# Optimization experiments

Measured on AMD Instinct MI355X. Metric: run time of the kernel, lower is better.

Reference implementation:

```python
import jax, jax.numpy as jnp
import numpy as np

C_IN, C_OUT, K = 64, 64, 3
KK = K * K


def _conv3x3(x, w, b):
    # x: [B, Cin, H, W], w: [Cout, Cin, 3, 3], b: [Cout] or None. stride 1, pad 1.
    y = jax.lax.conv_general_dilated(
        x, w, window_strides=(1, 1), padding=((1, 1), (1, 1)),
        dimension_numbers=("NCHW", "OIHW", "NCHW"))
    if b is not None:
        y = y + b[None, :, None, None]
    return y


def _deform_conv2d(x, offset, mask, weight):
    # torchvision.ops.deform_conv2d with stride=1, pad=1, dilation=1, 1 offset group.
    # x: [B,C,H,W]; offset: [B,2*KK,H,W] (per-tap (dy,dx)); mask: [B,KK,H,W];
    # weight: [O,C,K,K]
    B, C, H, W = x.shape
    O = weight.shape[0]
    ky, kx = jnp.meshgrid(jnp.arange(K), jnp.arange(K), indexing="ij")
    hs = jnp.arange(H)
    ws = jnp.arange(W)
    # base sample positions per tap k=(ky*K+kx): [KK,H,W]
    base_y = (hs[:, None] - 1)[None] + ky.reshape(KK, 1, 1)
    base_x = (ws[None, :] - 1)[None] + kx.reshape(KK, 1, 1)
    off = offset.reshape(B, KK, 2, H, W)
    py = base_y[None].astype(x.dtype) + off[:, :, 0]  # [B,KK,H,W]
    px = base_x[None].astype(x.dtype) + off[:, :, 1]

    y0 = jnp.floor(py)
    x0 = jnp.floor(px)
    wy = py - y0  # bilinear fractional weights
    wx = px - x0
    y0i = y0.astype(jnp.int32)
    x0i = x0.astype(jnp.int32)

    imflat = x.reshape(B, C, H * W)

    def gather_b(im, idx):  # im: [C,HW], idx: [KK,H,W] -> [C,KK,H,W]
        return im[:, idx]

    val = jnp.zeros((B, C, KK, H, W), x.dtype)
    for dy, dx in ((0, 0), (0, 1), (1, 0), (1, 1)):
        yc = y0i + dy
        xc = x0i + dx
        valid = ((yc >= 0) & (yc < H) & (xc >= 0) & (xc < W)).astype(x.dtype)
        cw = (wy if dy else (1.0 - wy)) * (wx if dx else (1.0 - wx)) * valid
        idx = jnp.clip(yc, 0, H - 1) * W + jnp.clip(xc, 0, W - 1)
        g = jax.vmap(gather_b)(imflat, idx)  # [B,C,KK,H,W]
        val = val + cw[:, None] * g
    val = val * mask[:, None]  # modulation
    # contract 9-tap patches with conv weight
    return jnp.einsum("bckhw,ock->bohw", val, weight.reshape(O, C, KK))


def setup_inputs() -> dict:
    key = jax.random.key(0)
    ks = jax.random.split(key, 8)
    B, H, W = 4, 96, 96
    cin2 = 2 * C_IN + 2
    frame_i = jax.random.normal(ks[0], (B, C_IN, H, W), jnp.float32)
    frame_j = jax.random.normal(ks[1], (B, C_IN, H, W), jnp.float32)
    flow_ij = jax.random.normal(ks[2], (B, 2, H, W), jnp.float32)
    # small random weights so offsets are nonzero (zero-init would degenerate)
    w_off = jax.random.normal(ks[3], (2 * KK, cin2, K, K), jnp.float32) * 0.01
    b_off = jax.random.normal(ks[4], (2 * KK,), jnp.float32) * 0.1
    w_mod = jax.random.normal(ks[5], (KK, cin2, K, K), jnp.float32) * 0.01
    b_mod = jax.random.normal(ks[6], (KK,), jnp.float32) * 0.1
    w_reg = jax.random.normal(ks[7], (C_OUT, C_IN, K, K), jnp.float32) * (1.0 / np.sqrt(C_IN * KK))
    return {"frame_i": frame_i, "frame_j": frame_j, "flow_ij": flow_ij,
            "w_off": w_off, "b_off": b_off, "w_mod": w_mod, "b_mod": b_mod,
            "w_reg": w_reg}


def reference(frame_i, frame_j, flow_ij, w_off, b_off, w_mod, b_mod, w_reg):
    offset_input = jnp.concatenate([frame_i, frame_j, flow_ij], axis=1)
    offset = _conv3x3(offset_input, w_off, b_off)            # [B,2*KK,H,W]
    modulator = 2.0 * jax.nn.sigmoid(_conv3x3(offset_input, w_mod, b_mod))  # [B,KK,H,W]
    return _deform_conv2d(frame_j, offset, modulator, w_reg)
```

## Files before the change

### kernel.cpp

```cpp
#include <hip/hip_runtime.h>
#include <math.h>

#define BB   4
#define HH   96
#define WW   96
#define HW   (HH * WW)
#define CIN  64
#define COUT 64
#define NPL  17
#define HWP  (HW + 1)
#define NROW (BB * HW)
#define NSTRIP (NROW / 16)
#define BPX3 (NSTRIP / 8)
#define NA   (9 * 5 * 2 * 512)
#define NW   (9 * 2 * 4 * 512)
#define PXB2 (NROW / 32)
#define PWBLK 324
#define TSX  35
#define NIT  (NPL * 54)

typedef short v8s __attribute__((ext_vector_type(8)));
typedef float v4f __attribute__((ext_vector_type(4)));

__device__ __forceinline__ unsigned short f2bf(float f) {
    unsigned u = __float_as_uint(f);
    return (unsigned short)((u + 0x7FFFu + ((u >> 16) & 1u)) >> 16);
}
__device__ __forceinline__ unsigned pack2(float a, float b) {
    return (unsigned)f2bf(a) | ((unsigned)f2bf(b) << 16);
}
__device__ __forceinline__ unsigned bil2(unsigned a, unsigned b, unsigned c,
                                         unsigned d, float w00, float w01,
                                         float w10, float w11) {
    float lo = w00 * __uint_as_float(a << 16) + w01 * __uint_as_float(b << 16)
             + w10 * __uint_as_float(c << 16) + w11 * __uint_as_float(d << 16);
    float hi = w00 * __uint_as_float(a & 0xffff0000u)
             + w01 * __uint_as_float(b & 0xffff0000u)
             + w10 * __uint_as_float(c & 0xffff0000u)
             + w11 * __uint_as_float(d & 0xffff0000u);
    return pack2(lo, hi);
}

__global__ __launch_bounds__(256) void prep_kernel(
    const float* __restrict__ fi, const float* __restrict__ fj,
    const float* __restrict__ fl, const float* __restrict__ w_off,
    const float* __restrict__ w_mod, const float* __restrict__ w_reg,
    uint4* __restrict__ xp, unsigned short* __restrict__ wa2f,
    unsigned short* __restrict__ wb2f)
{
    int blk = blockIdx.x;
    if (blk < PXB2) {
        __shared__ __align__(16) unsigned tile[64 * TSX];
        int tid = threadIdx.x;
        int p = tid & 63, cg = tid >> 6;
        int u = blk >> 1, half = blk & 1;
        int r0 = u * 64;
        int b = r0 / HW;
        int hwb = r0 - b * HW;
        int hw = hwb + p;
        uint4* xpb = xp + (size_t)b * NPL * HWP;
        if (half == 0) {
            const float* pi = fi + (size_t)b * CIN * HW + hw;
#pragma unroll
            for (int d = 0; d < 8; ++d) {
                int c = cg * 16 + 2 * d;
                tile[p * TSX + cg * 8 + d] =
                    pack2(pi[(size_t)c * HW], pi[(size_t)(c + 1) * HW]);
            }
            __syncthreads();
#pragma unroll
            for (int i = 0; i < 2; ++i) {
                int it = i * 256 + tid;
                int pl = it >> 6, rl = it & 63;
                const unsigned* s = &tile[rl * TSX + pl * 4];
                uint4 v = {s[0], s[1], s[2], s[3]};
                xpb[(size_t)pl * HWP + hwb + rl] = v;
            }
        } else {
            const float* pj = fj + (size_t)b * CIN * HW + hw;
#pragma unroll
            for (int d = 0; d < 8; ++d) {
                int c = cg * 16 + 2 * d;
                tile[p * TSX + cg * 8 + d] =
                    pack2(pj[(size_t)c * HW], pj[(size_t)(c + 1) * HW]);
            }
            if (cg == 0) {
                const float* pf = fl + (size_t)b * 2 * HW + hw;
                tile[p * TSX + 32] = pack2(pf[0], pf[HW]);
            }
            __syncthreads();
#pragma unroll
            for (int i = 0; i < 2; ++i) {
                int it = i * 256 + tid;
                int pl = it >> 6, rl = it & 63;
                int o  = (pl >> 1) + (pl & 1) * 4;
                const unsigned* s = &tile[rl * TSX + o * 4];
                uint4 v = {s[0], s[1], s[2], s[3]};
                xpb[(size_t)(8 + pl) * HWP + hwb + rl] = v;
            }
            if (tid < 64) {
                uint4 v = {tile[tid * TSX + 32], 0u, 0u, 0u};
                xpb[(size_t)16 * HWP + hwb + tid] = v;
            }
        }
    } else if (blk < PXB2 + PWBLK) {
        int e = (blk - PXB2) * 256 + threadIdx.x;
        if (e < NA) {
            int t  = e / 5120;
            int r1 = e - t * 5120;
            int ks = r1 >> 10;
            int r2 = r1 & 1023;
            int nt = r2 >> 9;
            int l9 = r2 & 511;
            int l  = l9 >> 3, ee = l9 & 7;
            int m  = l & 15, g = l >> 4;
            int oc = nt * 16 + m;
            int ch = ks * 32 + g * 8 + ee;
            float v = 0.0f;
            if (oc < 27 && ch < 130) {
                if (oc < 18) v = w_off[((size_t)oc * 130 + ch) * 9 + t];
                else         v = w_mod[((size_t)(oc - 18) * 130 + ch) * 9 + t];
            }
            wa2f[e] = f2bf(v);
        } else {
            int e2 = e - NA;
            if (e2 < NW) {
                int k  = e2 >> 12;
                int r1 = e2 & 4095;
                int ks = r1 >> 11;
                int r2 = r1 & 2047;
                int nt = r2 >> 9;
                int l9 = r2 & 511;
                int l  = l9 >> 3, ee = l9 & 7;
                int m  = l & 15, g = l >> 4;
                int o  = nt * 16 + m;
                int c  = ks * 32 + g * 8 + ee;
                wb2f[e2] = f2bf(w_reg[((size_t)o * 64 + c) * 9 + k]);
            }
        }
    } else {
        if (threadIdx.x < BB * NPL) {
            int bz = threadIdx.x / NPL, pl = threadIdx.x - bz * NPL;
            uint4 z = {0u, 0u, 0u, 0u};
            xp[((size_t)bz * NPL + pl) * HWP + HW] = z;
        }
    }
}

__global__ __launch_bounds__(512, 8) void fused_kernel(
    const uint4* __restrict__ xp,
    const unsigned short* __restrict__ wa2f,
    const unsigned short* __restrict__ wb2f,
    const float* __restrict__ b_off, const float* __restrict__ b_mod,
    float* __restrict__ out)
{
    __shared__ __align__(16) unsigned char pool[16384];
    __shared__ __align__(16) float red1[8][8][64];
    __shared__ float lraw[16 * 28];

    uint4* patchL = (uint4*)pool;
    float* red2   = (float*)pool;

    int tid = threadIdx.x;
    int l = tid & 63;
    int wid = __builtin_amdgcn_readfirstlane(tid >> 6);
    int m = l & 15, g = l >> 4;
    int strip = (blockIdx.x & 7) * BPX3 + (blockIdx.x >> 3);
    int b = strip / (HW / 16);
    int hw0 = (strip - b * (HW / 16)) * 16;
    int hw = hw0 + m;
    int x = hw % WW, y = hw / WW;
    int y0b = hw0 / WW, x0b = hw0 - y0b * WW;

    const uint4* xpb = xp + (size_t)b * NPL * HWP;

#pragma unroll
    for (int i = 0; i < 2; ++i) {
        int item = i * 512 + tid;
        if (item < NIT) {
            int pl  = item / 54;
            int rm  = item - pl * 54;
            int run = rm / 18;
            int r18 = rm - run * 18;
            int yy = y0b + run - 1;
            int xx = x0b - 1 + r18;
            bool ok = ((unsigned)yy < HH) && ((unsigned)xx < WW);
            int pos = ok ? (yy * WW + xx) : HW;
            patchL[item] = xpb[(size_t)pl * HWP + pos];
        }
    }
    __syncthreads();

    v4f acc0 = {0.f, 0.f, 0.f, 0.f};
    v4f acc1 = {0.f, 0.f, 0.f, 0.f};
    {
        int nu = (wid < 5) ? 6 : 5;
#pragma unroll
        for (int i = 0; i < 6; ++i) {
            if (i < nu) {
                int u = wid + 8 * i;
                int t = u / 5, ks = u - 5 * t;
                int r = (t / 3) * 18 + (t % 3) + m;
                v8s a;
                if (ks == 4) {
                    uint4 t4 = patchL[16 * 54 + r];
                    if (g) t4 = (uint4){0u, 0u, 0u, 0u};
                    a = __builtin_bit_cast(v8s, t4);
                } else {
                    int pl = (ks == 0) ? g : (ks == 1) ? 4 + g
                           : (ks == 2) ? 8 + 2 * g : 9 + 2 * g;
                    a = *(const v8s*)&patchL[pl * 54 + r];
                }
                const unsigned short* wp =
                    wa2f + ((size_t)(u * 2)) * 512 + l * 8;
                v8s b0 = *(const v8s*)(wp);
                v8s b1 = *(const v8s*)(wp + 512);
                acc0 = __builtin_amdgcn_mfma_f32_16x16x32_bf16(a, b0, acc0, 0, 0, 0);
                acc1 = __builtin_amdgcn_mfma_f32_16x16x32_bf16(a, b1, acc1, 0, 0, 0);
            }
        }
    }

    {
#pragma unroll
        for (int j = 0; j < 4; ++j) red1[wid][j][l] = acc0[j];
#pragma unroll
        for (int j = 0; j < 4; ++j) red1[wid][4 + j][l] = acc1[j];
    }
    __syncthreads();

    {
        int j = wid;
        float v = 0.f;
#pragma unroll
        for (int sw = 0; sw < 8; ++sw) v += red1[sw][j][l];
        int r = j & 3;
        int oc = (j < 4) ? m : 16 + m;
        int pos = g * 4 + r;
        if (oc < 18) {
            lraw[pos * 28 + oc] = v + b_off[oc];
        } else if (oc < 27) {
            lraw[pos * 28 + oc] =
                2.0f / (1.0f + __expf(-(v + b_mod[oc - 18])));
        }
    }
    __syncthreads();

    v4f acc[4];
#pragma unroll
    for (int nt = 0; nt < 4; ++nt) acc[nt] = (v4f){0.f, 0.f, 0.f, 0.f};

    auto do_tap = [&](int k) {
        int ky = k / 3, kx = k - 3 * ky;
        float dy = lraw[m * 28 + 2 * k];
        float dx = lraw[m * 28 + 2 * k + 1];
        float mm = lraw[m * 28 + 18 + k];

        float py = (float)(y - 1 + ky) + dy;
        float px = (float)(x - 1 + kx) + dx;
        float fy = floorf(py), fx = floorf(px);
        int   y0 = (int)fy,    x0 = (int)fx;
        float wy = py - fy,    wx = px - fx;
        int   y1 = y0 + 1,     x1 = x0 + 1;

        bool y0v = (y0 >= 0) && (y0 < HH);
        bool y1v = (y1 >= 0) && (y1 < HH);
        bool x0v = (x0 >= 0) && (x0 < WW);
        bool x1v = (x1 >= 0) && (x1 < WW);

        float w00 = (1.f - wy) * (1.f - wx) * ((y0v && x0v) ? mm : 0.f);
        float w01 = (1.f - wy) * wx         * ((y0v && x1v) ? mm : 0.f);
        float w10 = wy * (1.f - wx)         * ((y1v && x0v) ? mm : 0.f);
        float w11 = wy * wx                 * ((y1v && x1v) ? mm : 0.f);

        int y0c = min(max(y0, 0), HH - 1), y1c = min(max(y1, 0), HH - 1);
        int x0c = min(max(x0, 0), WW - 1), x1c = min(max(x1, 0), WW - 1);
        int i00 = y0c * WW + x0c, i01 = y0c * WW + x1c;
        int i10 = y1c * WW + x0c, i11 = y1c * WW + x1c;

        const uint4* p0 = xpb + (size_t)(8 + 2 * g) * HWP;
        const uint4* p1 = p0 + HWP;

        uint4 a00 = p0[i00];
        uint4 a01 = p0[i01];
        uint4 a10 = p0[i10];
        uint4 a11 = p0[i11];
        uint4 c00 = p1[i00];
        uint4 c01 = p1[i01];
        uint4 c10 = p1[i10];
        uint4 c11 = p1[i11];

        uint4 ov0, ov1;
        ov0.x = bil2(a00.x, a01.x, a10.x, a11.x, w00, w01, w10, w11);
        ov0.y = bil2(a00.y, a01.y, a10.y, a11.y, w00, w01, w10, w11);
        ov0.z = bil2(a00.z, a01.z, a10.z, a11.z, w00, w01, w10, w11);
        ov0.w = bil2(a00.w, a01.w, a10.w, a11.w, w00, w01, w10, w11);
        ov1.x = bil2(c00.x, c01.x, c10.x, c11.x, w00, w01, w10, w11);
        ov1.y = bil2(c00.y, c01.y, c10.y, c11.y, w00, w01, w10, w11);
        ov1.z = bil2(c00.z, c01.z, c10.z, c11.z, w00, w01, w10, w11);
        ov1.w = bil2(c00.w, c01.w, c10.w, c11.w, w00, w01, w10, w11);
        v8s af0 = __builtin_bit_cast(v8s, ov0);
        v8s af1 = __builtin_bit_cast(v8s, ov1);

#pragma unroll
        for (int nt = 0; nt < 4; ++nt) {
            const unsigned short* wp0 =
                wb2f + ((size_t)((k * 2 + 0) * 4 + nt)) * 512 + l * 8;
            const unsigned short* wp1 =
                wb2f + ((size_t)((k * 2 + 1) * 4 + nt)) * 512 + l * 8;
            v8s bb0 = *(const v8s*)wp0;
            v8s bb1 = *(const v8s*)wp1;
            acc[nt] = __builtin_amdgcn_mfma_f32_16x16x32_bf16(af0, bb0, acc[nt], 0, 0, 0);
            acc[nt] = __builtin_amdgcn_mfma_f32_16x16x32_bf16(af1, bb1, acc[nt], 0, 0, 0);
        }
    };

    auto do_half = [&](int k, int ks) {
        int ky = k / 3, kx = k - 3 * ky;
        float dy = lraw[m * 28 + 2 * k];
        float dx = lraw[m * 28 + 2 * k + 1];
        float mm = lraw[m * 28 + 18 + k];

        float py = (float)(y - 1 + ky) + dy;
        float px = (float)(x - 1 + kx) + dx;
        float fy = floorf(py), fx = floorf(px);
        int   y0 = (int)fy,    x0 = (int)fx;
        float wy = py - fy,    wx = px - fx;
        int   y1 = y0 + 1,     x1 = x0 + 1;

        bool y0v = (y0 >= 0) && (y0 < HH);
        bool y1v = (y1 >= 0) && (y1 < HH);
        bool x0v = (x0 >= 0) && (x0 < WW);
        bool x1v = (x1 >= 0) && (x1 < WW);

        float w00 = (1.f - wy) * (1.f - wx) * ((y0v && x0v) ? mm : 0.f);
        float w01 = (1.f - wy) * wx         * ((y0v && x1v) ? mm : 0.f);
        float w10 = wy * (1.f - wx)         * ((y1v && x0v) ? mm : 0.f);
        float w11 = wy * wx                 * ((y1v && x1v) ? mm : 0.f);

        int y0c = min(max(y0, 0), HH - 1), y1c = min(max(y1, 0), HH - 1);
        int x0c = min(max(x0, 0), WW - 1), x1c = min(max(x1, 0), WW - 1);
        int i00 = y0c * WW + x0c, i01 = y0c * WW + x1c;
        int i10 = y1c * WW + x0c, i11 = y1c * WW + x1c;

        const uint4* pk = xpb + (size_t)(8 + 2 * g + ks) * HWP;
        uint4 a00 = pk[i00];
        uint4 a01 = pk[i01];
        uint4 a10 = pk[i10];
        uint4 a11 = pk[i11];

        uint4 ov;
        ov.x = bil2(a00.x, a01.x, a10.x, a11.x, w00, w01, w10, w11);
        ov.y = bil2(a00.y, a01.y, a10.y, a11.y, w00, w01, w10, w11);
        ov.z = bil2(a00.z, a01.z, a10.z, a11.z, w00, w01, w10, w11);
        ov.w = bil2(a00.w, a01.w, a10.w, a11.w, w00, w01, w10, w11);
        v8s af = __builtin_bit_cast(v8s, ov);

#pragma unroll
        for (int nt = 0; nt < 4; ++nt) {
            const unsigned short* wp =
                wb2f + ((size_t)((k * 2 + ks) * 4 + nt)) * 512 + l * 8;
            v8s bb = *(const v8s*)wp;
            acc[nt] = __builtin_amdgcn_mfma_f32_16x16x32_bf16(af, bb, acc[nt], 0, 0, 0);
        }
    };

    do_tap(wid);
    if (wid == 6) do_half(8, 0);
    if (wid == 7) do_half(8, 1);

    if (wid >= 4) {
        float* rb = red2 + ((size_t)(wid - 4) * 16) * 64;
#pragma unroll
        for (int nt = 0; nt < 4; ++nt)
#pragma unroll
            for (int r = 0; r < 4; ++r)
                rb[(nt * 4 + r) * 64 + l] = acc[nt][r];
    }
    __syncthreads();
    if (wid < 4) {
        float* rb = red2 + ((size_t)wid * 16) * 64;
#pragma unroll
        for (int nt = 0; nt < 4; ++nt)
#pragma unroll
            for (int r = 0; r < 4; ++r) {
                float t = rb[(nt * 4 + r) * 64 + l] + acc[nt][r];
                rb[(nt * 4 + r) * 64 + l] = t;
            }
    }
    __syncthreads();
    {
        int nt = wid >> 1, r0 = (wid & 1) * 2;
        float v0 = 0.f, v1 = 0.f;
#pragma unroll
        for (int bu = 0; bu < 4; ++bu) {
            v0 += red2[((size_t)bu * 16 + nt * 4 + r0) * 64 + l];
            v1 += red2[((size_t)bu * 16 + nt * 4 + r0 + 1) * 64 + l];
        }
        float* op = out + ((size_t)(b * COUT + nt * 16 + m)) * HW
                  + hw0 + g * 4 + r0;
        float2 s2 = {v0, v1};
        *(float2*)op = s2;
    }
}

extern "C" void kernel_launch(void* const* d_in, const int* in_sizes, int n_in,
                              void* d_out, int out_size, void* d_ws, size_t ws_size,
                              hipStream_t stream)
{
    const float* frame_i = (const float*)d_in[0];
    const float* frame_j = (const float*)d_in[1];
    const float* flow_ij = (const float*)d_in[2];
    const float* w_off   = (const float*)d_in[3];
    const float* b_off   = (const float*)d_in[4];
    const float* w_mod   = (const float*)d_in[5];
    const float* b_mod   = (const float*)d_in[6];
    const float* w_reg   = (const float*)d_in[7];
    float* out = (float*)d_out;

    uint4* xp = (uint4*)d_ws;
    unsigned short* wa2f = (unsigned short*)(xp + (size_t)BB * NPL * HWP);
    unsigned short* wb2f = wa2f + NA;

    prep_kernel<<<PXB2 + PWBLK + 1, 256, 0, stream>>>(
        frame_i, frame_j, flow_ij, w_off, w_mod, w_reg, xp, wa2f, wb2f);

    fused_kernel<<<NSTRIP, 512, 0, stream>>>(
        xp, wa2f, wb2f, b_off, b_mod, out);
}
```

Baseline: 112.1 us.

## Process 32 pixels per block to reuse weight fragments across two M-tiles

```diff
diff --git a/kernel.cpp b/kernel.cpp
--- a/kernel.cpp
+++ b/kernel.cpp
@@ -10,14 +10,15 @@
 #define NPL  17
 #define HWP  (HW + 1)
 #define NROW (BB * HW)
-#define NSTRIP (NROW / 16)
-#define BPX3 (NSTRIP / 8)
+#define MPB  32
+#define NBLK (NROW / MPB)
+#define BPX4 (NBLK / 8)
 #define NA   (9 * 5 * 2 * 512)
 #define NW   (9 * 2 * 4 * 512)
 #define PXB2 (NROW / 32)
 #define PWBLK 324
 #define TSX  35
-#define NIT  (NPL * 54)
+#define NIT2 (NPL * 102)
 
 typedef short v8s __attribute__((ext_vector_type(8)));
 typedef float v4f __attribute__((ext_vector_type(4)));
@@ -147,16 +148,16 @@
     }
 }
 
-__global__ __launch_bounds__(512, 8) void fused_kernel(
+__global__ __launch_bounds__(512, 4) void fused_kernel(
     const uint4* __restrict__ xp,
     const unsigned short* __restrict__ wa2f,
     const unsigned short* __restrict__ wb2f,
     const float* __restrict__ b_off, const float* __restrict__ b_mod,
     float* __restrict__ out)
 {
-    __shared__ __align__(16) unsigned char pool[16384];
-    __shared__ __align__(16) float red1[8][8][64];
-    __shared__ float lraw[16 * 28];
+    __shared__ __align__(16) unsigned char pool[32768];
+    __shared__ __align__(16) float red1[4][16][64];
+    __shared__ float lraw[32 * 28];
 
     uint4* patchL = (uint4*)pool;
     float* red2   = (float*)pool;
@@ -165,25 +166,25 @@
     int l = tid & 63;
     int wid = __builtin_amdgcn_readfirstlane(tid >> 6);
     int m = l & 15, g = l >> 4;
-    int strip = (blockIdx.x & 7) * BPX3 + (blockIdx.x >> 3);
-    int b = strip / (HW / 16);
-    int hw0 = (strip - b * (HW / 16)) * 16;
-    int hw = hw0 + m;
-    int x = hw % WW, y = hw / WW;
-    int y0b = hw0 / WW, x0b = hw0 - y0b * WW;
+    int blkid = (blockIdx.x & 7) * BPX4 + (blockIdx.x >> 3);
+    int b = blkid / (HW / MPB);
+    int rem = blkid - b * (HW / MPB);
+    int y = rem / 3;
+    int x0b = (rem - y * 3) * 32;
+    int hw0 = y * WW + x0b;
 
     const uint4* xpb = xp + (size_t)b * NPL * HWP;
 
 #pragma unroll
-    for (int i = 0; i < 2; ++i) {
+    for (int i = 0; i < 4; ++i) {
         int item = i * 512 + tid;
-        if (item < NIT) {
-            int pl  = item / 54;
-            int rm  = item - pl * 54;
-            int run = rm / 18;
-            int r18 = rm - run * 18;
-            int yy = y0b + run - 1;
-            int xx = x0b - 1 + r18;
+        if (item < NIT2) {
+            int pl  = item / 102;
+            int rm  = item - pl * 102;
+            int run = rm / 34;
+            int c34 = rm - run * 34;
+            int yy = y + run - 1;
+            int xx = x0b - 1 + c34;
             bool ok = ((unsigned)yy < HH) && ((unsigned)xx < WW);
             int pos = ok ? (yy * WW + xx) : HW;
             patchL[item] = xpb[(size_t)pl * HWP + pos];
@@ -191,8 +192,10 @@
     }
     __syncthreads();
 
-    v4f acc0 = {0.f, 0.f, 0.f, 0.f};
-    v4f acc1 = {0.f, 0.f, 0.f, 0.f};
+    v4f acc00 = {0.f, 0.f, 0.f, 0.f};
+    v4f acc01 = {0.f, 0.f, 0.f, 0.f};
+    v4f acc10 = {0.f, 0.f, 0.f, 0.f};
+    v4f acc11 = {0.f, 0.f, 0.f, 0.f};
     {
         int nu = (wid < 5) ? 6 : 5;
 #pragma unroll
@@ -200,64 +203,94 @@
             if (i < nu) {
                 int u = wid + 8 * i;
                 int t = u / 5, ks = u - 5 * t;
-                int r = (t / 3) * 18 + (t % 3) + m;
-                v8s a;
+                int run = t / 3, kx = t - 3 * run;
+                int rb = run * 34 + kx + m;
+                v8s a0, a1;
                 if (ks == 4) {
-                    uint4 t4 = patchL[16 * 54 + r];
-                    if (g) t4 = (uint4){0u, 0u, 0u, 0u};
-                    a = __builtin_bit_cast(v8s, t4);
+                    uint4 t0 = patchL[16 * 102 + rb];
+                    uint4 t1 = patchL[16 * 102 + rb + 16];
+                    if (g) { t0 = (uint4){0u,0u,0u,0u}; t1 = (uint4){0u,0u,0u,0u}; }
+                    a0 = __builtin_bit_cast(v8s, t0);
+                    a1 = __builtin_bit_cast(v8s, t1);
                 } else {
                     int pl = (ks == 0) ? g : (ks == 1) ? 4 + g
                            : (ks == 2) ? 8 + 2 * g : 9 + 2 * g;
-                    a = *(const v8s*)&patchL[pl * 54 + r];
+                    a0 = *(const v8s*)&patchL[pl * 102 + rb];
+                    a1 = *(const v8s*)&patchL[pl * 102 + rb + 16];
                 }
                 const unsigned short* wp =
                     wa2f + ((size_t)(u * 2)) * 512 + l * 8;
                 v8s b0 = *(const v8s*)(wp);
                 v8s b1 = *(const v8s*)(wp + 512);
-                acc0 = __builtin_amdgcn_mfma_f32_16x16x32_bf16(a, b0, acc0, 0, 0, 0);
-                acc1 = __builtin_amdgcn_mfma_f32_16x16x32_bf16(a, b1, acc1, 0, 0, 0);
-            }
-        }
-    }
+                acc00 = __builtin_amdgcn_mfma_f32_16x16x32_bf16(a0, b0, acc00, 0, 0, 0);
+                acc01 = __builtin_amdgcn_mfma_f32_16x16x32_bf16(a0, b1, acc01, 0, 0, 0);
+                acc10 = __builtin_amdgcn_mfma_f32_16x16x32_bf16(a1, b0, acc10, 0, 0, 0);
+                acc11 = __builtin_amdgcn_mfma_f32_16x16x32_bf16(a1, b1, acc11, 0, 0, 0);
+            }
+        }
+    }
+
+    if (wid >= 4) {
+        float* rb = &red1[wid - 4][0][0];
+#pragma unroll
+        for (int j = 0; j < 4; ++j) {
+            rb[(0 + j) * 64 + l]  = acc00[j];
+            rb[(4 + j) * 64 + l]  = acc01[j];
+            rb[(8 + j) * 64 + l]  = acc10[j];
+            rb[(12 + j) * 64 + l] = acc11[j];
+        }
+    }
+    __syncthreads();
+    if (wid < 4) {
+        float* rb = &red1[wid][0][0];
+#pragma unroll
+        for (int j = 0; j < 4; ++j) {
+            rb[(0 + j) * 64 + l]  += acc00[j];
+            rb[(4 + j) * 64 + l]  += acc01[j];
+            rb[(8 + j) * 64 + l]  += acc10[j];
+            rb[(12 + j) * 64 + l] += acc11[j];
+        }
+    }
+    __syncthreads();
 
     {
 #pragma unroll
-        for (int j = 0; j < 4; ++j) red1[wid][j][l] = acc0[j];
-#pragma unroll
-        for (int j = 0; j < 4; ++j) red1[wid][4 + j][l] = acc1[j];
-    }
-    __syncthreads();
-
-    {
-        int j = wid;
-        float v = 0.f;
-#pragma unroll
-        for (int sw = 0; sw < 8; ++sw) v += red1[sw][j][l];
-        int r = j & 3;
-        int oc = (j < 4) ? m : 16 + m;
-        int pos = g * 4 + r;
-        if (oc < 18) {
-            lraw[pos * 28 + oc] = v + b_off[oc];
-        } else if (oc < 27) {
-            lraw[pos * 28 + oc] =
-                2.0f / (1.0f + __expf(-(v + b_mod[oc - 18])));
-        }
-    }
-    __syncthreads();
-
-    v4f acc[4];
-#pragma unroll
-    for (int nt = 0; nt < 4; ++nt) acc[nt] = (v4f){0.f, 0.f, 0.f, 0.f};
-
-    auto do_tap = [&](int k) {
+        for (int ss = 0; ss < 2; ++ss) {
+            int s = wid * 2 + ss;
+            int q = s >> 3, j = s & 7;
+            float v = red1[0][s][l] + red1[1][s][l]
+                    + red1[2][s][l] + red1[3][s][l];
+            int r = j & 3;
+            int oc = (j < 4) ? m : 16 + m;
+            int pos = q * 16 + g * 4 + r;
+            if (oc < 18) {
+                lraw[pos * 28 + oc] = v + b_off[oc];
+            } else if (oc < 27) {
+                lraw[pos * 28 + oc] =
+                    2.0f / (1.0f + __expf(-(v + b_mod[oc - 18])));
+            }
+        }
+    }
+    __syncthreads();
+
+    v4f acc2[2][4];
+#pragma unroll
+    for (int q = 0; q < 2; ++q)
+#pragma unroll
+        for (int nt = 0; nt < 4; ++nt) acc2[q][nt] = (v4f){0.f, 0.f, 0.f, 0.f};
+
+    const uint4* p0 = xpb + (size_t)(8 + 2 * g) * HWP;
+    const uint4* p1 = p0 + HWP;
+
+    auto mk_af = [&](int k, int q, v8s& af0, v8s& af1) {
         int ky = k / 3, kx = k - 3 * ky;
-        float dy = lraw[m * 28 + 2 * k];
-        float dx = lraw[m * 28 + 2 * k + 1];
-        float mm = lraw[m * 28 + 18 + k];
+        int pos = q * 16 + m;
+        float dy = lraw[pos * 28 + 2 * k];
+        float dx = lraw[pos * 28 + 2 * k + 1];
+        float mm = lraw[pos * 28 + 18 + k];
 
         float py = (float)(y - 1 + ky) + dy;
-        float px = (float)(x - 1 + kx) + dx;
+        float px = (float)(x0b + pos - 1 + kx) + dx;
         float fy = floorf(py), fx = floorf(px);
         int   y0 = (int)fy,    x0 = (int)fx;
         float wy = py - fy,    wx = px - fx;
@@ -277,9 +310,6 @@
         int x0c = min(max(x0, 0), WW - 1), x1c = min(max(x1, 0), WW - 1);
         int i00 = y0c * WW + x0c, i01 = y0c * WW + x1c;
         int i10 = y1c * WW + x0c, i11 = y1c * WW + x1c;
-
-        const uint4* p0 = xpb + (size_t)(8 + 2 * g) * HWP;
-        const uint4* p1 = p0 + HWP;
 
         uint4 a00 = p0[i00];
         uint4 a01 = p0[i01];
@@ -299,9 +329,14 @@
         ov1.y = bil2(c00.y, c01.y, c10.y, c11.y, w00, w01, w10, w11);
         ov1.z = bil2(c00.z, c01.z, c10.z, c11.z, w00, w01, w10, w11);
         ov1.w = bil2(c00.w, c01.w, c10.w, c11.w, w00, w01, w10, w11);
-        v8s af0 = __builtin_bit_cast(v8s, ov0);
-        v8s af1 = __builtin_bit_cast(v8s, ov1);
-
+        af0 = __builtin_bit_cast(v8s, ov0);
+        af1 = __builtin_bit_cast(v8s, ov1);
+    };
+
+    auto do_tap = [&](int k) {
+        v8s af[2][2];
+        mk_af(k, 0, af[0][0], af[0][1]);
+        mk_af(k, 1, af[1][0], af[1][1]);
 #pragma unroll
         for (int nt = 0; nt < 4; ++nt) {
             const unsigned short* wp0 =
@@ -310,58 +345,65 @@
                 wb2f + ((size_t)((k * 2 + 1) * 4 + nt)) * 512 + l * 8;
             v8s bb0 = *(const v8s*)wp0;
             v8s bb1 = *(const v8s*)wp1;
-            acc[nt] = __builtin_amdgcn_mfma_f32_16x16x32_bf16(af0, bb0, acc[nt], 0, 0, 0);
-            acc[nt] = __builtin_amdgcn_mfma_f32_16x16x32_bf16(af1, bb1, acc[nt], 0, 0, 0);
+            acc2[0][nt] = __builtin_amdgcn_mfma_f32_16x16x32_bf16(af[0][0], bb0, acc2[0][nt], 0, 0, 0);
+            acc2[0][nt] = __builtin_amdgcn_mfma_f32_16x16x32_bf16(af[0][1], bb1, acc2[0][nt], 0, 0, 0);
+            acc2[1][nt] = __builtin_amdgcn_mfma_f32_16x16x32_bf16(af[1][0], bb0, acc2[1][nt], 0, 0, 0);
+            acc2[1][nt] = __builtin_amdgcn_mfma_f32_16x16x32_bf16(af[1][1], bb1, acc2[1][nt], 0, 0, 0);
         }
     };
 
     auto do_half = [&](int k, int ks) {
-        int ky = k / 3, kx = k - 3 * ky;
-        float dy = lraw[m * 28 + 2 * k];
-        float dx = lraw[m * 28 + 2 * k + 1];
-        float mm = lraw[m * 28 + 18 + k];
-
-        float py = (float)(y - 1 + ky) + dy;
-        float px = (float)(x - 1 + kx) + dx;
-        float fy = floorf(py), fx = floorf(px);
-        int   y0 = (int)fy,    x0 = (int)fx;
-        float wy = py - fy,    wx = px - fx;
-        int   y1 = y0 + 1,     x1 = x0 + 1;
-
-        bool y0v = (y0 >= 0) && (y0 < HH);
-        bool y1v = (y1 >= 0) && (y1 < HH);
-        bool x0v = (x0 >= 0) && (x0 < WW);
-        bool x1v = (x1 >= 0) && (x1 < WW);
-
-        float w00 = (1.f - wy) * (1.f - wx) * ((y0v && x0v) ? mm : 0.f);
-        float w01 = (1.f - wy) * wx         * ((y0v && x1v) ? mm : 0.f);
-        float w10 = wy * (1.f - wx)         * ((y1v && x0v) ? mm : 0.f);
-        float w11 = wy * wx                 * ((y1v && x1v) ? mm : 0.f);
-
-        int y0c = min(max(y0, 0), HH - 1), y1c = min(max(y1, 0), HH - 1);
-        int x0c = min(max(x0, 0), WW - 1), x1c = min(max(x1, 0), WW - 1);
-        int i00 = y0c * WW + x0c, i01 = y0c * WW + x1c;
-        int i10 = y1c * WW + x0c, i11 = y1c * WW + x1c;
-
-        const uint4* pk = xpb + (size_t)(8 + 2 * g + ks) * HWP;
-        uint4 a00 = pk[i00];
-        uint4 a01 = pk[i01];
-        uint4 a10 = pk[i10];
-        uint4 a11 = pk[i11];
-
-        uint4 ov;
-        ov.x = bil2(a00.x, a01.x, a10.x, a11.x, w00, w01, w10, w11);
-        ov.y = bil2(a00.y, a01.y, a10.y, a11.y, w00, w01, w10, w11);
-        ov.z = bil2(a00.z, a01.z, a10.z, a11.z, w00, w01, w10, w11);
-        ov.w = bil2(a00.w, a01.w, a10.w, a11.w, w00, w01, w10, w11);
-        v8s af = __builtin_bit_cast(v8s, ov);
-
+        v8s af[2];
+#pragma unroll
+        for (int q = 0; q < 2; ++q) {
+            int ky = k / 3, kx = k - 3 * ky;
+            int pos = q * 16 + m;
+            float dy = lraw[pos * 28 + 2 * k];
+            float dx = lraw[pos * 28 + 2 * k + 1];
+            float mm = lraw[pos * 28 + 18 + k];
+
+            float py = (float)(y - 1 + ky) + dy;
+            float px = (float)(x0b + pos - 1 + kx) + dx;
+            float fy = floorf(py), fx = floorf(px);
+            int   y0 = (int)fy,    x0 = (int)fx;
+            float wy = py - fy,    wx = px - fx;
+            int   y1 = y0 + 1,     x1 = x0 + 1;
+
+            bool y0v = (y0 >= 0) && (y0 < HH);
+            bool y1v = (y1 >= 0) && (y1 < HH);
+            bool x0v = (x0 >= 0) && (x0 < WW);
+            bool x1v = (x1 >= 0) && (x1 < WW);
+
+            float w00 = (1.f - wy) * (1.f - wx) * ((y0v && x0v) ? mm : 0.f);
+            float w01 = (1.f - wy) * wx         * ((y0v && x1v) ? mm : 0.f);
+            float w10 = wy * (1.f - wx)         * ((y1v && x0v) ? mm : 0.f);
+            float w11 = wy * wx                 * ((y1v && x1v) ? mm : 0.f);
+
+            int y0c = min(max(y0, 0), HH - 1), y1c = min(max(y1, 0), HH - 1);
+            int x0c = min(max(x0, 0), WW - 1), x1c = min(max(x1, 0), WW - 1);
+            int i00 = y0c * WW + x0c, i01 = y0c * WW + x1c;
+            int i10 = y1c * WW + x0c, i11 = y1c * WW + x1c;
+
+            const uint4* pk = xpb + (size_t)(8 + 2 * g + ks) * HWP;
+            uint4 a00 = pk[i00];
+            uint4 a01 = pk[i01];
+            uint4 a10 = pk[i10];
+            uint4 a11 = pk[i11];
+
+            uint4 ov;
+            ov.x = bil2(a00.x, a01.x, a10.x, a11.x, w00, w01, w10, w11);
+            ov.y = bil2(a00.y, a01.y, a10.y, a11.y, w00, w01, w10, w11);
+            ov.z = bil2(a00.z, a01.z, a10.z, a11.z, w00, w01, w10, w11);
+            ov.w = bil2(a00.w, a01.w, a10.w, a11.w, w00, w01, w10, w11);
+            af[q] = __builtin_bit_cast(v8s, ov);
+        }
 #pragma unroll
         for (int nt = 0; nt < 4; ++nt) {
             const unsigned short* wp =
                 wb2f + ((size_t)((k * 2 + ks) * 4 + nt)) * 512 + l * 8;
             v8s bb = *(const v8s*)wp;
-            acc[nt] = __builtin_amdgcn_mfma_f32_16x16x32_bf16(af, bb, acc[nt], 0, 0, 0);
+            acc2[0][nt] = __builtin_amdgcn_mfma_f32_16x16x32_bf16(af[0], bb, acc2[0][nt], 0, 0, 0);
+            acc2[1][nt] = __builtin_amdgcn_mfma_f32_16x16x32_bf16(af[1], bb, acc2[1][nt], 0, 0, 0);
         }
     };
 
@@ -369,38 +411,45 @@
     if (wid == 6) do_half(8, 0);
     if (wid == 7) do_half(8, 1);
 
+    __syncthreads();
     if (wid >= 4) {
-        float* rb = red2 + ((size_t)(wid - 4) * 16) * 64;
-#pragma unroll
-        for (int nt = 0; nt < 4; ++nt)
-#pragma unroll
-            for (int r = 0; r < 4; ++r)
-                rb[(nt * 4 + r) * 64 + l] = acc[nt][r];
+        float* rb = red2 + ((size_t)(wid - 4) * 32) * 64;
+#pragma unroll
+        for (int q = 0; q < 2; ++q)
+#pragma unroll
+            for (int nt = 0; nt < 4; ++nt)
+#pragma unroll
+                for (int r = 0; r < 4; ++r)
+                    rb[(q * 16 + nt * 4 + r) * 64 + l] = acc2[q][nt][r];
     }
     __syncthreads();
     if (wid < 4) {
-        float* rb = red2 + ((size_t)wid * 16) * 64;
-#pragma unroll
-        for (int nt = 0; nt < 4; ++nt)
-#pragma unroll
-            for (int r = 0; r < 4; ++r) {
-                float t = rb[(nt * 4 + r) * 64 + l] + acc[nt][r];
-                rb[(nt * 4 + r) * 64 + l] = t;
-            }
+        float* rb = red2 + ((size_t)wid * 32) * 64;
+#pragma unroll
+        for (int q = 0; q < 2; ++q)
+#pragma unroll
+            for (int nt = 0; nt < 4; ++nt)
+#pragma unroll
+                for (int r = 0; r < 4; ++r) {
+                    float t = rb[(q * 16 + nt * 4 + r) * 64 + l] + acc2[q][nt][r];
+                    rb[(q * 16 + nt * 4 + r) * 64 + l] = t;
+                }
     }
     __syncthreads();
     {
-        int nt = wid >> 1, r0 = (wid & 1) * 2;
-        float v0 = 0.f, v1 = 0.f;
-#pragma unroll
-        for (int bu = 0; bu < 4; ++bu) {
-            v0 += red2[((size_t)bu * 16 + nt * 4 + r0) * 64 + l];
-            v1 += red2[((size_t)bu * 16 + nt * 4 + r0 + 1) * 64 + l];
+        int q = wid >> 2, nt = wid & 3;
+        v4f s = {0.f, 0.f, 0.f, 0.f};
+#pragma unroll
+        for (int r = 0; r < 4; ++r) {
+            float t = 0.f;
+#pragma unroll
+            for (int bu = 0; bu < 4; ++bu)
+                t += red2[((size_t)bu * 32 + q * 16 + nt * 4 + r) * 64 + l];
+            s[r] = t;
         }
         float* op = out + ((size_t)(b * COUT + nt * 16 + m)) * HW
-                  + hw0 + g * 4 + r0;
-        float2 s2 = {v0, v1};
-        *(float2*)op = s2;
+                  + hw0 + q * 16 + g * 4;
+        *(v4f*)op = s;
     }
 }
 
@@ -425,6 +474,6 @@
     prep_kernel<<<PXB2 + PWBLK + 1, 256, 0, stream>>>(
         frame_i, frame_j, flow_ij, w_off, w_mod, w_reg, xp, wa2f, wb2f);
 
-    fused_kernel<<<NSTRIP, 512, 0, stream>>>(
+    fused_kernel<<<NBLK, 512, 0, stream>>>(
         xp, wa2f, wb2f, b_off, b_mod, out);
 }
```

After: 114.9 us. +2.5%, slower.
